# Kernel tuning notes

Measured on AMD Instinct MI355X. Metric: run time of the kernel, lower is better.

Reference implementation:

```python
import jax, jax.numpy as jnp
import numpy as np

U = 8192        # unique source nodes this hop
E = 200000      # candidate paths (edges)
D = 768         # node feature dim (== hidden, GIN residual requires it)
DE = 50         # edge one-hot dim
O = 768         # output dim
BN_EPS = 1e-5


def setup_inputs() -> dict:
    key = jax.random.key(0)
    ks = jax.random.split(key, 10)
    inp = {
        "x_src_unique": jax.random.normal(ks[0], (U, D), dtype=jnp.float32),
        "unique_src_to_process_indices": jnp.arange(U, dtype=jnp.int64),
        "path_source_indices_global": jax.random.randint(ks[1], (E,), 0, U).astype(jnp.int64),
        "path_target_node_features": jax.random.normal(ks[2], (E, D), dtype=jnp.float32),
        "path_edge_features": jax.random.normal(ks[3], (E, DE), dtype=jnp.float32),
        # edge_transform_linear: Linear(D+DE, H) with bias
        "W_edge": jax.random.normal(ks[4], (D, D + DE), dtype=jnp.float32) * (1.0 / np.sqrt(D + DE)),
        "b_edge": jnp.zeros((D,), dtype=jnp.float32),
        # MLP: two bias-free linears with BatchNorm1d between
        "W1": jax.random.normal(ks[5], (D, D), dtype=jnp.float32) * (1.0 / np.sqrt(D)),
        "W2": jax.random.normal(ks[6], (O, D), dtype=jnp.float32) * (1.0 / np.sqrt(D)),
        "bn_gamma": jnp.ones((D,), dtype=jnp.float32),
        "bn_beta": jnp.zeros((D,), dtype=jnp.float32),
        "eps_param": jnp.zeros((1,), dtype=jnp.float32),  # GIN eps (init_eps=0)
    }
    return inp


def reference(x_src_unique, unique_src_to_process_indices, path_source_indices_global,
              path_target_node_features, path_edge_features,
              W_edge, b_edge, W1, W2, bn_gamma, bn_beta, eps_param):
    # map global source ids -> local rows of x_src_unique (unique ids are sorted)
    local_idx = jnp.searchsorted(unique_src_to_process_indices, path_source_indices_global)

    # per-path message: relu(Linear([h_tgt ; e_onehot]))  -> [E, H]
    msg_in = jnp.concatenate([path_target_node_features, path_edge_features], axis=-1)
    msgs = jax.nn.relu(msg_in @ W_edge.T + b_edge)

    # scatter-sum messages to their source node  -> [U, H]
    agg = jax.ops.segment_sum(msgs, local_idx, num_segments=x_src_unique.shape[0])

    # GIN combine + MLP (BatchNorm1d in training mode, batch > 1)
    h = (1.0 + eps_param[0]) * x_src_unique + agg
    h1 = h @ W1.T                               # [U, H]
    mean = jnp.mean(h1, axis=0)
    var = jnp.var(h1, axis=0)                   # biased, matches torch BN normalization
    h1 = (h1 - mean) * jax.lax.rsqrt(var + BN_EPS) * bn_gamma + bn_beta
    h1 = jax.nn.relu(h1)
    return h1 @ W2.T                            # [U, O]
```

## Files before the change

kernel.cpp:

```cpp
#include <hip/hip_runtime.h>
#include <stdint.h>
#include <math.h>

typedef unsigned short u16;
typedef __attribute__((ext_vector_type(4))) float f32x4;
typedef __attribute__((ext_vector_type(8))) short s16x8;
typedef __attribute__((ext_vector_type(4))) int i32x4;

#define U_N 8192
#define E_N 200000
#define M_PAD 200192
#define D_N 768
#define DE_N 50
#define KP8 896
#define NTI8 7
#define BN_EPS 1e-5f

__device__ __forceinline__ u16 f2bf(float f) {
  union { float f; unsigned u; } v; v.f = f;
  return (u16)((v.u + 0x7fffu + ((v.u >> 16) & 1u)) >> 16);
}
__device__ __forceinline__ float bf2f(u16 v) {
  union { unsigned u; float f; } x; x.u = ((unsigned)v) << 16; return x.f;
}
__device__ __forceinline__ void gload16(const void* g, void* l) {
  __builtin_amdgcn_global_load_lds((const __attribute__((address_space(1))) void*)g,
                                   (__attribute__((address_space(3))) void*)l, 16, 0, 0);
}

__global__ void k_localidx(const int* __restrict__ uniq, const int* __restrict__ src,
                           int* __restrict__ lidx) {
  int e = blockIdx.x * 256 + threadIdx.x;
  if (e >= E_N) return;
  int v = src[e];
  int lo = 0, hi = U_N;
  while (lo < hi) { int mid = (lo + hi) >> 1; if (uniq[mid] < v) lo = mid + 1; else hi = mid; }
  lidx[e] = lo;
}

__global__ void k_hist(const int* __restrict__ lidx, int* __restrict__ counts) {
  int e = blockIdx.x * 256 + threadIdx.x;
  if (e < E_N) atomicAdd(&counts[lidx[e]], 1);
}

__global__ void k_scan(const int* __restrict__ counts, int* __restrict__ starts) {
  __shared__ int part[1024];
  const int t = threadIdx.x;
  const int base = t * 8;
  int loc[8]; int s = 0;
#pragma unroll
  for (int i = 0; i < 8; i++) { loc[i] = s; s += counts[base + i]; }
  part[t] = s; __syncthreads();
  for (int off = 1; off < 1024; off <<= 1) {
    int v = (t >= off) ? part[t - off] : 0;
    __syncthreads();
    part[t] += v;
    __syncthreads();
  }
  const int pre = (t == 0) ? 0 : part[t - 1];
#pragma unroll
  for (int i = 0; i < 8; i++) starts[base + i] = pre + loc[i];
  if (t == 1023) starts[8192] = pre + s;
}

__global__ void k_scatter(const int* __restrict__ lidx, const int* __restrict__ starts,
                          int* __restrict__ cursor, int* __restrict__ eord,
                          int* __restrict__ nsort) {
  int e = blockIdx.x * 256 + threadIdx.x;
  if (e >= E_N) return;
  int u = lidx[e];
  int pos = atomicAdd(&cursor[u], 1);
  eord[starts[u] + pos] = e;
  nsort[starts[u] + pos] = u;
}

__global__ __launch_bounds__(256)
void k_pack_q8(const float* __restrict__ tgt, const float* __restrict__ edg,
               const int* __restrict__ eord, char* __restrict__ Aq,
               float* __restrict__ sA) {
  const int row = blockIdx.x * 4 + (threadIdx.x >> 6);
  const int lane = threadIdx.x & 63;
  if (row >= E_N) return;
  const int e = eord[row];
  const int k0 = lane * 16;
  float v[16];
#pragma unroll
  for (int z = 0; z < 16; z++) v[z] = 0.f;
  if (k0 < D_N) {
    const f32x4* p = (const f32x4*)(tgt + (size_t)e * D_N + k0);
#pragma unroll
    for (int zz = 0; zz < 4; zz++) {
      const f32x4 f = p[zz];
#pragma unroll
      for (int b = 0; b < 4; b++) v[zz * 4 + b] = f[b];
    }
  } else if (k0 < KP8) {
#pragma unroll
    for (int z = 0; z < 16; z++) {
      const int kk = k0 + z - D_N;
      v[z] = (kk < DE_N) ? edg[(size_t)e * DE_N + kk] : 0.f;
    }
  }
  float am = 0.f;
#pragma unroll
  for (int z = 0; z < 16; z++) am = fmaxf(am, fabsf(v[z]));
#pragma unroll
  for (int off = 32; off > 0; off >>= 1) am = fmaxf(am, __shfl_xor(am, off));
  am = fmaxf(am, 1e-8f);
  const float inv = 127.f / am;
  if (lane == 0) sA[row] = am / 127.f;
  if (k0 < KP8) {
    int wq[4];
#pragma unroll
    for (int zz = 0; zz < 4; zz++) {
      int b0 = (int)rintf(fminf(fmaxf(v[zz*4+0] * inv, -127.f), 127.f));
      int b1 = (int)rintf(fminf(fmaxf(v[zz*4+1] * inv, -127.f), 127.f));
      int b2 = (int)rintf(fminf(fmaxf(v[zz*4+2] * inv, -127.f), 127.f));
      int b3 = (int)rintf(fminf(fmaxf(v[zz*4+3] * inv, -127.f), 127.f));
      wq[zz] = (b0 & 255) | ((b1 & 255) << 8) | ((b2 & 255) << 16) | (b3 << 24);
    }
    i32x4 out = {wq[0], wq[1], wq[2], wq[3]};
    *(i32x4*)(Aq + (size_t)row * KP8 + k0) = out;
  }
}

__global__ __launch_bounds__(256)
void k_convw_q8(const float* __restrict__ W, char* __restrict__ Wq,
                float* __restrict__ sW) {
  const int row = blockIdx.x * 4 + (threadIdx.x >> 6);
  const int lane = threadIdx.x & 63;
  if (row >= D_N) return;
  const int k0 = lane * 16;
  float v[16];
#pragma unroll
  for (int z = 0; z < 16; z++) v[z] = 0.f;
  if (k0 < KP8) {
#pragma unroll
    for (int z = 0; z < 16; z++) {
      const int kk = k0 + z;
      v[z] = (kk < D_N + DE_N) ? W[(size_t)row * (D_N + DE_N) + kk] : 0.f;
    }
  }
  float am = 0.f;
#pragma unroll
  for (int z = 0; z < 16; z++) am = fmaxf(am, fabsf(v[z]));
#pragma unroll
  for (int off = 32; off > 0; off >>= 1) am = fmaxf(am, __shfl_xor(am, off));
  am = fmaxf(am, 1e-8f);
  const float inv = 127.f / am;
  if (lane == 0) sW[row] = am / 127.f;
  if (k0 < KP8) {
    int wq[4];
#pragma unroll
    for (int zz = 0; zz < 4; zz++) {
      int b0 = (int)rintf(fminf(fmaxf(v[zz*4+0] * inv, -127.f), 127.f));
      int b1 = (int)rintf(fminf(fmaxf(v[zz*4+1] * inv, -127.f), 127.f));
      int b2 = (int)rintf(fminf(fmaxf(v[zz*4+2] * inv, -127.f), 127.f));
      int b3 = (int)rintf(fminf(fmaxf(v[zz*4+3] * inv, -127.f), 127.f));
      wq[zz] = (b0 & 255) | ((b1 & 255) << 8) | ((b2 & 255) << 16) | (b3 << 24);
    }
    i32x4 out = {wq[0], wq[1], wq[2], wq[3]};
    *(i32x4*)(Wq + (size_t)row * KP8 + k0) = out;
  }
}

__global__ void k_conv_w(const float* __restrict__ W, u16* __restrict__ Wb, int count) {
  int i = blockIdx.x * 256 + threadIdx.x;
  if (i < count) Wb[i] = f2bf(W[i]);
}

__global__ __launch_bounds__(512)
void gemm_edge8(const char* __restrict__ Aq, const char* __restrict__ Wq,
                const float* __restrict__ sA, const float* __restrict__ sW,
                const float* __restrict__ bias, const int* __restrict__ nsort,
                float* __restrict__ agg) {
  __shared__ char lds[139264];

  const int orig = blockIdx.x;
  const int xcd = orig & 7, i8_ = orig >> 3;
  const int wgid = (xcd < 2 ? xcd * 294 : 588 + (xcd - 2) * 293) + i8_;
  const int bm = (wgid / 3) * 256;
  const int bn = (wgid % 3) * 256;

  const int tid = threadIdx.x;
  const int w = tid >> 6, lane = tid & 63;
  const int wm = w >> 2, wn = w & 3;
  const int rl = lane & 15, K16 = lane >> 4;
  const int srr = lane >> 3;
  const int ssrc = (lane & 7) ^ srr;

  i32x4 acc[8][4] = {};

#define STAGE8(T)                                                                       \
  {                                                                                     \
    const int b_ = (T) & 1;                                                             \
    const int k0_ = (T) * 128;                                                          \
    _Pragma("unroll")                                                                   \
    for (int c_ = 0; c_ < 4; ++c_) {                                                    \
      const int cc_ = c_ * 8 + w;                                                       \
      const int r_ = cc_ * 8 + srr;                                                     \
      gload16(Aq + (size_t)(bm + r_) * KP8 + k0_ + ssrc * 16, lds + b_ * 32768 + cc_ * 1024); \
    }                                                                                   \
    _Pragma("unroll")                                                                   \
    for (int c_ = 0; c_ < 4; ++c_) {                                                    \
      const int cc_ = c_ * 8 + w;                                                       \
      const int r_ = cc_ * 8 + srr;                                                     \
      gload16(Wq + (size_t)(bn + r_) * KP8 + k0_ + ssrc * 16, lds + 65536 + b_ * 32768 + cc_ * 1024); \
    }                                                                                   \
  }

#define COMPUTE_H(BB, h_)                                                               \
  {                                                                                     \
    const char* Ab = lds + (BB) * 32768;                                                \
    const char* Bb = lds + 65536 + (BB) * 32768;                                        \
    const int sb_ = (h_) * 4 + K16;                                                     \
    const int sw_ = (sb_ ^ (rl & 7)) * 16;                                              \
    i32x4 bfr[4], af[4];                                                                \
    _Pragma("unroll")                                                                   \
    for (int j_ = 0; j_ < 4; ++j_)                                                      \
      bfr[j_] = *(const i32x4*)(Bb + (wn * 64 + j_ * 16 + rl) * 128 + sw_);             \
    _Pragma("unroll")                                                                   \
    for (int i_ = 0; i_ < 4; ++i_)                                                      \
      af[i_] = *(const i32x4*)(Ab + (wm * 128 + i_ * 16 + rl) * 128 + sw_);             \
    __builtin_amdgcn_s_setprio(1);                                                      \
    _Pragma("unroll")                                                                   \
    for (int i_ = 0; i_ < 4; ++i_)                                                      \
      _Pragma("unroll")                                                                 \
      for (int j_ = 0; j_ < 4; ++j_)                                                    \
        acc[i_][j_] = __builtin_amdgcn_mfma_i32_16x16x64_i8(af[i_], bfr[j_],            \
                                                            acc[i_][j_], 0, 0, 0);     \
    __builtin_amdgcn_s_setprio(0);                                                      \
    _Pragma("unroll")                                                                   \
    for (int i_ = 0; i_ < 4; ++i_)                                                      \
      af[i_] = *(const i32x4*)(Ab + (wm * 128 + (4 + i_) * 16 + rl) * 128 + sw_);       \
    __builtin_amdgcn_s_setprio(1);                                                      \
    _Pragma("unroll")                                                                   \
    for (int i_ = 0; i_ < 4; ++i_)                                                      \
      _Pragma("unroll")                                                                 \
      for (int j_ = 0; j_ < 4; ++j_)                                                    \
        acc[4 + i_][j_] = __builtin_amdgcn_mfma_i32_16x16x64_i8(af[i_], bfr[j_],        \
                                                                acc[4 + i_][j_], 0, 0, 0); \
    __builtin_amdgcn_s_setprio(0);                                                      \
  }

#define VMC(n)  asm volatile("s_waitcnt vmcnt(" #n ")" ::: "memory")
#define BAR()   __builtin_amdgcn_s_barrier()

  STAGE8(0)
  for (int t = 0; t < NTI8 - 1; ++t) {
    BAR();
    STAGE8(t + 1)
    VMC(8);
    BAR();
    asm volatile("" ::: "memory");
    COMPUTE_H(t & 1, 0)
    COMPUTE_H(t & 1, 1)
  }
  BAR();
  VMC(0);
  BAR();
  asm volatile("" ::: "memory");
  COMPUTE_H(0, 0)
  COMPUTE_H(0, 1)

#undef STAGE8
#undef COMPUTE_H

  BAR();

  u16* tile = (u16*)lds;
  int* nseg = (int*)(lds + 137216);
  float* sAl = (float*)(lds + 138240);
  for (int i = tid; i < 256; i += 512) {
    nseg[i] = nsort[bm + i];
    sAl[i] = sA[bm + i];
  }
  __syncthreads();

  const int rq = (lane >> 4) * 4;
  const int cl = lane & 15;
#pragma unroll
  for (int j = 0; j < 4; ++j) {
    const int col16 = wn * 64 + j * 16 + cl;
    const float swn = sW[bn + col16];
    const float bj = bias[bn + col16];
#pragma unroll
    for (int mf = 0; mf < 8; ++mf) {
      const int r0 = wm * 128 + mf * 16 + rq;
#pragma unroll
      for (int q = 0; q < 4; ++q) {
        const int r = r0 + q;
        const float v = fmaf((float)acc[mf][j][q], sAl[r] * swn, bj);
        tile[r * 268 + col16] = f2bf(v > 0.f ? v : 0.f);
      }
    }
  }
  __syncthreads();

  const int col = tid & 255;
  const int rbase = (tid >> 8) * 128;
  float s = 0.f;
  int cur = -1;
  for (int r = 0; r < 128; ++r) {
    const int nd = nseg[rbase + r];
    const float v = bf2f(tile[(rbase + r) * 268 + col]);
    if (nd != cur) {
      if (cur >= 0) atomicAdd(&agg[(size_t)cur * D_N + bn + col], s);
      s = 0.f;
      cur = nd;
    }
    if (nd >= 0) s += v;
  }
  if (cur >= 0) atomicAdd(&agg[(size_t)cur * D_N + bn + col], s);

#undef VMC
#undef BAR
}

__global__ void k_build_h(const float* __restrict__ x, const float* __restrict__ agg,
                          const float* __restrict__ epsp, u16* __restrict__ hbf) {
  int i = blockIdx.x * 256 + threadIdx.x;
  if (i >= U_N * D_N) return;
  float h = (1.f + epsp[0]) * x[i] + agg[i];
  hbf[i] = f2bf(h);
}

__global__ __launch_bounds__(256)
void gemm_h1(const u16* __restrict__ A, const u16* __restrict__ B,
             u16* __restrict__ h1b, float* __restrict__ ssum, float* __restrict__ ssq) {
  __shared__ u16 As[128 * 64];
  __shared__ u16 Bs[128 * 64];
  const int bm = (blockIdx.x / 6) * 128;
  const int bn = (blockIdx.x % 6) * 128;
  const int t = threadIdx.x;
  const int wave = t >> 6, lane = t & 63;
  const int wr = (wave & 1) * 64, wc = (wave >> 1) * 64;
  const int srow = lane >> 3, scol = (lane & 7) * 8;
  const int rl = lane & 15, kl = (lane >> 4) * 8;
  f32x4 acc[4][4] = {};
  for (int k0 = 0; k0 < D_N; k0 += 64) {
#pragma unroll
    for (int q = 0; q < 4; q++) {
      const int c = wave * 4 + q;
      const int row = c * 8 + srow;
      gload16(A + (size_t)(bm + row) * D_N + k0 + scol, As + c * 512);
      gload16(B + (size_t)(bn + row) * D_N + k0 + scol, Bs + c * 512);
    }
    __syncthreads();
#pragma unroll
    for (int ks = 0; ks < 2; ks++) {
      s16x8 af[4], bfr[4];
#pragma unroll
      for (int i = 0; i < 4; i++) af[i] = *(const s16x8*)&As[(wr + i * 16 + rl) * 64 + ks * 32 + kl];
#pragma unroll
      for (int j = 0; j < 4; j++) bfr[j] = *(const s16x8*)&Bs[(wc + j * 16 + rl) * 64 + ks * 32 + kl];
#pragma unroll
      for (int i = 0; i < 4; i++)
#pragma unroll
        for (int j = 0; j < 4; j++)
          acc[i][j] = __builtin_amdgcn_mfma_f32_16x16x32_bf16(af[i], bfr[j], acc[i][j], 0, 0, 0);
    }
    __syncthreads();
  }
  const int cl = lane & 15, rq = (lane >> 4) * 4;
#pragma unroll
  for (int j = 0; j < 4; j++) {
    const int n = bn + wc + j * 16 + cl;
    float cs = 0.f, cq = 0.f;
#pragma unroll
    for (int i = 0; i < 4; i++) {
      const int r = bm + wr + i * 16 + rq;
#pragma unroll
      for (int q = 0; q < 4; q++) {
        const float v = acc[i][j][q];
        cs += v; cq += v * v;
        h1b[(size_t)(r + q) * D_N + n] = f2bf(v);
      }
    }
    cs += __shfl_xor(cs, 16); cq += __shfl_xor(cq, 16);
    cs += __shfl_xor(cs, 32); cq += __shfl_xor(cq, 32);
    if (lane < 16) { atomicAdd(&ssum[n], cs); atomicAdd(&ssq[n], cq); }
  }
}

__global__ __launch_bounds__(256)
void gemm_bf16_g(const u16* __restrict__ A, const u16* __restrict__ B,
                 float* __restrict__ C, int ntn, int K) {
  __shared__ u16 As[128 * 64];
  __shared__ u16 Bs[128 * 64];
  const int bm = (blockIdx.x / ntn) * 128;
  const int bn = (blockIdx.x % ntn) * 128;
  const int t = threadIdx.x;
  const int wave = t >> 6, lane = t & 63;
  const int wr = (wave & 1) * 64, wc = (wave >> 1) * 64;
  const int srow = lane >> 3, scol = (lane & 7) * 8;
  const int rl = lane & 15, kl = (lane >> 4) * 8;
  const int N = ntn * 128;
  f32x4 acc[4][4] = {};
  for (int k0 = 0; k0 < K; k0 += 64) {
#pragma unroll
    for (int q = 0; q < 4; q++) {
      const int c = wave * 4 + q;
      const int row = c * 8 + srow;
      gload16(A + (size_t)(bm + row) * K + k0 + scol, As + c * 512);
      gload16(B + (size_t)(bn + row) * K + k0 + scol, Bs + c * 512);
    }
    __syncthreads();
#pragma unroll
    for (int ks = 0; ks < 2; ks++) {
      s16x8 af[4], bfr[4];
#pragma unroll
      for (int i = 0; i < 4; i++) af[i] = *(const s16x8*)&As[(wr + i * 16 + rl) * 64 + ks * 32 + kl];
#pragma unroll
      for (int j = 0; j < 4; j++) bfr[j] = *(const s16x8*)&Bs[(wc + j * 16 + rl) * 64 + ks * 32 + kl];
#pragma unroll
      for (int i = 0; i < 4; i++)
#pragma unroll
        for (int j = 0; j < 4; j++)
          acc[i][j] = __builtin_amdgcn_mfma_f32_16x16x32_bf16(af[i], bfr[j], acc[i][j], 0, 0, 0);
    }
    __syncthreads();
  }
  const int cl = lane & 15, rq = (lane >> 4) * 4;
#pragma unroll
  for (int i = 0; i < 4; i++)
#pragma unroll
    for (int j = 0; j < 4; j++) {
      const int n = bn + wc + j * 16 + cl;
      const int r = bm + wr + i * 16 + rq;
#pragma unroll
      for (int q = 0; q < 4; q++)
        C[(size_t)(r + q) * N + n] = acc[i][j][q];
    }
}

__global__ void k_bnfinal(const float* __restrict__ ssum, const float* __restrict__ ssq,
                          const float* __restrict__ gamma, const float* __restrict__ beta,
                          float* __restrict__ scale, float* __restrict__ shift) {
  int c = blockIdx.x * 256 + threadIdx.x;
  if (c >= D_N) return;
  double mean = (double)ssum[c] / (double)U_N;
  double var = (double)ssq[c] / (double)U_N - mean * mean;
  float sc = (float)((double)gamma[c] / sqrt(var + (double)BN_EPS));
  scale[c] = sc;
  shift[c] = beta[c] - (float)mean * sc;
}

__global__ void k_bnapply(const u16* __restrict__ h1b, const float* __restrict__ scale,
                          const float* __restrict__ shift, u16* __restrict__ h2) {
  int i = blockIdx.x * 256 + threadIdx.x;
  if (i >= U_N * D_N) return;
  int c = i % D_N;
  float v = bf2f(h1b[i]) * scale[c] + shift[c];
  h2[i] = f2bf(v > 0.f ? v : 0.f);
}

extern "C" void kernel_launch(void* const* d_in, const int* in_sizes, int n_in,
                              void* d_out, int out_size, void* d_ws, size_t ws_size,
                              hipStream_t stream) {
  const float* x     = (const float*)d_in[0];
  const int*   uniq  = (const int*)d_in[1];
  const int*   srcg  = (const int*)d_in[2];
  const float* tgt   = (const float*)d_in[3];
  const float* edg   = (const float*)d_in[4];
  const float* Wedge = (const float*)d_in[5];
  const float* bedge = (const float*)d_in[6];
  const float* W1    = (const float*)d_in[7];
  const float* W2    = (const float*)d_in[8];
  const float* gamma = (const float*)d_in[9];
  const float* beta  = (const float*)d_in[10];
  const float* epsp  = (const float*)d_in[11];
  float* out = (float*)d_out;
  char* ws = (char*)d_ws;

  char*  Aq    = (char*) (ws + 0);
  float* agg   = (float*)(ws + 179372032ull);
  u16*   h1b   = (u16*)  (ws + 204537856ull);
  u16*   hbf   = (u16*)  (ws + 217120768ull);
  u16*   h2b   = (u16*)  (ws + 229703680ull);
  char*  Wq    = (char*) (ws + 242286592ull);
  u16*   w1b   = (u16*)  (ws + 242974720ull);
  u16*   w2b   = (u16*)  (ws + 244154368ull);
  float* sA    = (float*)(ws + 245334016ull);
  float* sW    = (float*)(ws + 246134784ull);
  int*   lidx  = (int*)  (ws + 246138880ull);
  int*   eord  = (int*)  (ws + 246938880ull);
  int*   nsort = (int*)  (ws + 247738880ull);
  int*   counts= (int*)  (ws + 248539648ull);
  int*   cursor= (int*)  (ws + 248572416ull);
  int*   starts= (int*)  (ws + 248605184ull);
  float* ssum  = (float*)(ws + 248638208ull);
  float* ssq   = (float*)(ws + 248641280ull);
  float* scale = (float*)(ws + 248644352ull);
  float* shift = (float*)(ws + 248647424ull);

  hipMemsetAsync(counts, 0, 65536, stream);
  hipMemsetAsync(ssum, 0, 2 * D_N * 4, stream);
  hipMemsetAsync(agg, 0, (size_t)U_N * D_N * 4, stream);
  hipMemsetAsync(nsort + E_N, 0xFF, (M_PAD - E_N) * 4, stream);

  k_convw_q8<<<D_N / 4, 256, 0, stream>>>(Wedge, Wq, sW);
  k_conv_w<<<(D_N * D_N + 255) / 256, 256, 0, stream>>>(W1, w1b, D_N * D_N);
  k_conv_w<<<(D_N * D_N + 255) / 256, 256, 0, stream>>>(W2, w2b, D_N * D_N);

  k_localidx<<<(E_N + 255) / 256, 256, 0, stream>>>(uniq, srcg, lidx);
  k_hist<<<(E_N + 255) / 256, 256, 0, stream>>>(lidx, counts);
  k_scan<<<1, 1024, 0, stream>>>(counts, starts);
  k_scatter<<<(E_N + 255) / 256, 256, 0, stream>>>(lidx, starts, cursor, eord, nsort);

  k_pack_q8<<<E_N / 4, 256, 0, stream>>>(tgt, edg, eord, Aq, sA);

  gemm_edge8<<<782 * 3, 512, 0, stream>>>(Aq, Wq, sA, sW, bedge, nsort, agg);

  k_build_h<<<(U_N * D_N + 255) / 256, 256, 0, stream>>>(x, agg, epsp, hbf);

  gemm_h1<<<(U_N / 128) * 6, 256, 0, stream>>>(hbf, w1b, h1b, ssum, ssq);

  k_bnfinal<<<3, 256, 0, stream>>>(ssum, ssq, gamma, beta, scale, shift);
  k_bnapply<<<(U_N * D_N + 255) / 256, 256, 0, stream>>>(h1b, scale, shift, h2b);

  gemm_bf16_g<<<(U_N / 128) * 6, 256, 0, stream>>>(h2b, w2b, out, 6, D_N);
}
```

Before: 569.1 us.

## Retile int8 edge GEMM to 128x128x64 with K padded to 832, fuse small kernels

```diff
diff --git a/kernel.cpp b/kernel.cpp
--- a/kernel.cpp
+++ b/kernel.cpp
@@ -9,11 +9,12 @@
 
 #define U_N 8192
 #define E_N 200000
-#define M_PAD 200192
+#define M_PAD 200064
+#define NMT 1563
 #define D_N 768
 #define DE_N 50
-#define KP8 896
-#define NTI8 7
+#define KP_E 832
+#define NTI 13
 #define BN_EPS 1e-5f
 
 __device__ __forceinline__ u16 f2bf(float f) {
@@ -28,19 +29,15 @@
                                    (__attribute__((address_space(3))) void*)l, 16, 0, 0);
 }
 
-__global__ void k_localidx(const int* __restrict__ uniq, const int* __restrict__ src,
-                           int* __restrict__ lidx) {
+__global__ void k_lh(const int* __restrict__ uniq, const int* __restrict__ src,
+                     int* __restrict__ lidx, int* __restrict__ counts) {
   int e = blockIdx.x * 256 + threadIdx.x;
   if (e >= E_N) return;
   int v = src[e];
   int lo = 0, hi = U_N;
   while (lo < hi) { int mid = (lo + hi) >> 1; if (uniq[mid] < v) lo = mid + 1; else hi = mid; }
   lidx[e] = lo;
-}
-
-__global__ void k_hist(const int* __restrict__ lidx, int* __restrict__ counts) {
-  int e = blockIdx.x * 256 + threadIdx.x;
-  if (e < E_N) atomicAdd(&counts[lidx[e]], 1);
+  atomicAdd(&counts[lo], 1);
 }
 
 __global__ void k_scan(const int* __restrict__ counts, int* __restrict__ starts) {
@@ -94,7 +91,7 @@
 #pragma unroll
       for (int b = 0; b < 4; b++) v[zz * 4 + b] = f[b];
     }
-  } else if (k0 < KP8) {
+  } else if (k0 < KP_E) {
 #pragma unroll
     for (int z = 0; z < 16; z++) {
       const int kk = k0 + z - D_N;
@@ -109,7 +106,7 @@
   am = fmaxf(am, 1e-8f);
   const float inv = 127.f / am;
   if (lane == 0) sA[row] = am / 127.f;
-  if (k0 < KP8) {
+  if (k0 < KP_E) {
     int wq[4];
 #pragma unroll
     for (int zz = 0; zz < 4; zz++) {
@@ -120,7 +117,7 @@
       wq[zz] = (b0 & 255) | ((b1 & 255) << 8) | ((b2 & 255) << 16) | (b3 << 24);
     }
     i32x4 out = {wq[0], wq[1], wq[2], wq[3]};
-    *(i32x4*)(Aq + (size_t)row * KP8 + k0) = out;
+    *(i32x4*)(Aq + (size_t)row * KP_E + k0) = out;
   }
 }
 
@@ -134,7 +131,7 @@
   float v[16];
 #pragma unroll
   for (int z = 0; z < 16; z++) v[z] = 0.f;
-  if (k0 < KP8) {
+  if (k0 < KP_E) {
 #pragma unroll
     for (int z = 0; z < 16; z++) {
       const int kk = k0 + z;
@@ -149,7 +146,7 @@
   am = fmaxf(am, 1e-8f);
   const float inv = 127.f / am;
   if (lane == 0) sW[row] = am / 127.f;
-  if (k0 < KP8) {
+  if (k0 < KP_E) {
     int wq[4];
 #pragma unroll
     for (int zz = 0; zz < 4; zz++) {
@@ -160,68 +157,65 @@
       wq[zz] = (b0 & 255) | ((b1 & 255) << 8) | ((b2 & 255) << 16) | (b3 << 24);
     }
     i32x4 out = {wq[0], wq[1], wq[2], wq[3]};
-    *(i32x4*)(Wq + (size_t)row * KP8 + k0) = out;
-  }
-}
-
-__global__ void k_conv_w(const float* __restrict__ W, u16* __restrict__ Wb, int count) {
+    *(i32x4*)(Wq + (size_t)row * KP_E + k0) = out;
+  }
+}
+
+__global__ void k_conv_w2(const float* __restrict__ W1, const float* __restrict__ W2,
+                          u16* __restrict__ w1b, u16* __restrict__ w2b) {
   int i = blockIdx.x * 256 + threadIdx.x;
-  if (i < count) Wb[i] = f2bf(W[i]);
-}
-
-__global__ __launch_bounds__(512)
-void gemm_edge8(const char* __restrict__ Aq, const char* __restrict__ Wq,
+  const int C = D_N * D_N;
+  if (i < C) w1b[i] = f2bf(W1[i]);
+  else if (i < 2 * C) w2b[i - C] = f2bf(W2[i - C]);
+}
+
+__global__ __launch_bounds__(256, 4)
+void gemm_edge9(const char* __restrict__ Aq, const char* __restrict__ Wq,
                 const float* __restrict__ sA, const float* __restrict__ sW,
                 const float* __restrict__ bias, const int* __restrict__ nsort,
                 float* __restrict__ agg) {
-  __shared__ char lds[139264];
+  __shared__ char lds[34816];
 
   const int orig = blockIdx.x;
   const int xcd = orig & 7, i8_ = orig >> 3;
-  const int wgid = (xcd < 2 ? xcd * 294 : 588 + (xcd - 2) * 293) + i8_;
-  const int bm = (wgid / 3) * 256;
-  const int bn = (wgid % 3) * 256;
+  const int wgid = (xcd < 2 ? xcd * 1173 : 2346 + (xcd - 2) * 1172) + i8_;
+  const int bm = (wgid / 6) * 128;
+  const int bn = (wgid % 6) * 128;
 
   const int tid = threadIdx.x;
   const int w = tid >> 6, lane = tid & 63;
-  const int wm = w >> 2, wn = w & 3;
+  const int wm = w & 1, wn = w >> 1;
   const int rl = lane & 15, K16 = lane >> 4;
-  const int srr = lane >> 3;
-  const int ssrc = (lane & 7) ^ srr;
-
-  i32x4 acc[8][4] = {};
-
-#define STAGE8(T)                                                                       \
+  const int sws = (K16 ^ ((rl >> 1) & 3)) * 16;
+  const int srow = tid >> 2;
+  const int sg0 = (tid & 3) ^ ((srow >> 1) & 3);
+
+  i32x4 acc[4][4] = {};
+
+#define VMC(n)  asm volatile("s_waitcnt vmcnt(" #n ")" ::: "memory")
+#define BAR()   __builtin_amdgcn_s_barrier()
+
+#define STAGE9(T)                                                                       \
   {                                                                                     \
     const int b_ = (T) & 1;                                                             \
-    const int k0_ = (T) * 128;                                                          \
-    _Pragma("unroll")                                                                   \
-    for (int c_ = 0; c_ < 4; ++c_) {                                                    \
-      const int cc_ = c_ * 8 + w;                                                       \
-      const int r_ = cc_ * 8 + srr;                                                     \
-      gload16(Aq + (size_t)(bm + r_) * KP8 + k0_ + ssrc * 16, lds + b_ * 32768 + cc_ * 1024); \
-    }                                                                                   \
-    _Pragma("unroll")                                                                   \
-    for (int c_ = 0; c_ < 4; ++c_) {                                                    \
-      const int cc_ = c_ * 8 + w;                                                       \
-      const int r_ = cc_ * 8 + srr;                                                     \
-      gload16(Wq + (size_t)(bn + r_) * KP8 + k0_ + ssrc * 16, lds + 65536 + b_ * 32768 + cc_ * 1024); \
-    }                                                                                   \
-  }
-
-#define COMPUTE_H(BB, h_)                                                               \
+    const int k0_ = (T) * 64;                                                           \
+    gload16(Aq + (size_t)(bm + srow) * KP_E + k0_ + sg0 * 16, lds + b_ * 16384 + tid * 16); \
+    gload16(Aq + (size_t)(bm + srow + 64) * KP_E + k0_ + sg0 * 16, lds + b_ * 16384 + 4096 + tid * 16); \
+    gload16(Wq + (size_t)(bn + srow) * KP_E + k0_ + sg0 * 16, lds + b_ * 16384 + 8192 + tid * 16); \
+    gload16(Wq + (size_t)(bn + srow + 64) * KP_E + k0_ + sg0 * 16, lds + b_ * 16384 + 12288 + tid * 16); \
+  }
+
+#define COMPUTE9(BB)                                                                    \
   {                                                                                     \
-    const char* Ab = lds + (BB) * 32768;                                                \
-    const char* Bb = lds + 65536 + (BB) * 32768;                                        \
-    const int sb_ = (h_) * 4 + K16;                                                     \
-    const int sw_ = (sb_ ^ (rl & 7)) * 16;                                              \
-    i32x4 bfr[4], af[4];                                                                \
+    const char* Ab = lds + (BB) * 16384;                                                \
+    const char* Bb = Ab + 8192;                                                         \
+    i32x4 af[4], bfr[4];                                                                \
     _Pragma("unroll")                                                                   \
     for (int j_ = 0; j_ < 4; ++j_)                                                      \
-      bfr[j_] = *(const i32x4*)(Bb + (wn * 64 + j_ * 16 + rl) * 128 + sw_);             \
+      bfr[j_] = *(const i32x4*)(Bb + (wn * 64 + j_ * 16 + rl) * 64 + sws);              \
     _Pragma("unroll")                                                                   \
     for (int i_ = 0; i_ < 4; ++i_)                                                      \
-      af[i_] = *(const i32x4*)(Ab + (wm * 128 + i_ * 16 + rl) * 128 + sw_);             \
+      af[i_] = *(const i32x4*)(Ab + (wm * 64 + i_ * 16 + rl) * 64 + sws);               \
     __builtin_amdgcn_s_setprio(1);                                                      \
     _Pragma("unroll")                                                                   \
     for (int i_ = 0; i_ < 4; ++i_)                                                      \
@@ -230,48 +224,32 @@
         acc[i_][j_] = __builtin_amdgcn_mfma_i32_16x16x64_i8(af[i_], bfr[j_],            \
                                                             acc[i_][j_], 0, 0, 0);     \
     __builtin_amdgcn_s_setprio(0);                                                      \
-    _Pragma("unroll")                                                                   \
-    for (int i_ = 0; i_ < 4; ++i_)                                                      \
-      af[i_] = *(const i32x4*)(Ab + (wm * 128 + (4 + i_) * 16 + rl) * 128 + sw_);       \
-    __builtin_amdgcn_s_setprio(1);                                                      \
-    _Pragma("unroll")                                                                   \
-    for (int i_ = 0; i_ < 4; ++i_)                                                      \
-      _Pragma("unroll")                                                                 \
-      for (int j_ = 0; j_ < 4; ++j_)                                                    \
-        acc[4 + i_][j_] = __builtin_amdgcn_mfma_i32_16x16x64_i8(af[i_], bfr[j_],        \
-                                                                acc[4 + i_][j_], 0, 0, 0); \
-    __builtin_amdgcn_s_setprio(0);                                                      \
-  }
-
-#define VMC(n)  asm volatile("s_waitcnt vmcnt(" #n ")" ::: "memory")
-#define BAR()   __builtin_amdgcn_s_barrier()
-
-  STAGE8(0)
-  for (int t = 0; t < NTI8 - 1; ++t) {
+  }
+
+  STAGE9(0)
+  for (int t = 0; t < NTI - 1; ++t) {
     BAR();
-    STAGE8(t + 1)
-    VMC(8);
+    STAGE9(t + 1)
+    VMC(4);
     BAR();
     asm volatile("" ::: "memory");
-    COMPUTE_H(t & 1, 0)
-    COMPUTE_H(t & 1, 1)
+    COMPUTE9(t & 1)
   }
   BAR();
   VMC(0);
   BAR();
   asm volatile("" ::: "memory");
-  COMPUTE_H(0, 0)
-  COMPUTE_H(0, 1)
-
-#undef STAGE8
-#undef COMPUTE_H
+  COMPUTE9(0)
+
+#undef STAGE9
+#undef COMPUTE9
 
   BAR();
 
   u16* tile = (u16*)lds;
-  int* nseg = (int*)(lds + 137216);
-  float* sAl = (float*)(lds + 138240);
-  for (int i = tid; i < 256; i += 512) {
+  int* nseg = (int*)(lds + 33792);
+  float* sAl = (float*)(lds + 34304);
+  for (int i = tid; i < 128; i += 256) {
     nseg[i] = nsort[bm + i];
     sAl[i] = sA[bm + i];
   }
@@ -285,25 +263,25 @@
     const float swn = sW[bn + col16];
     const float bj = bias[bn + col16];
 #pragma unroll
-    for (int mf = 0; mf < 8; ++mf) {
-      const int r0 = wm * 128 + mf * 16 + rq;
+    for (int i = 0; i < 4; ++i) {
+      const int r0 = wm * 64 + i * 16 + rq;
 #pragma unroll
       for (int q = 0; q < 4; ++q) {
         const int r = r0 + q;
-        const float v = fmaf((float)acc[mf][j][q], sAl[r] * swn, bj);
-        tile[r * 268 + col16] = f2bf(v > 0.f ? v : 0.f);
+        const float v = fmaf((float)acc[i][j][q], sAl[r] * swn, bj);
+        tile[r * 132 + col16] = f2bf(v > 0.f ? v : 0.f);
       }
     }
   }
   __syncthreads();
 
-  const int col = tid & 255;
-  const int rbase = (tid >> 8) * 128;
+  const int col = tid & 127;
+  const int rbase = (tid >> 7) * 64;
   float s = 0.f;
   int cur = -1;
-  for (int r = 0; r < 128; ++r) {
+  for (int r = 0; r < 64; ++r) {
     const int nd = nseg[rbase + r];
-    const float v = bf2f(tile[(rbase + r) * 268 + col]);
+    const float v = bf2f(tile[(rbase + r) * 132 + col]);
     if (nd != cur) {
       if (cur >= 0) atomicAdd(&agg[(size_t)cur * D_N + bn + col], s);
       s = 0.f;
@@ -474,25 +452,25 @@
   char* ws = (char*)d_ws;
 
   char*  Aq    = (char*) (ws + 0);
-  float* agg   = (float*)(ws + 179372032ull);
-  u16*   h1b   = (u16*)  (ws + 204537856ull);
-  u16*   hbf   = (u16*)  (ws + 217120768ull);
-  u16*   h2b   = (u16*)  (ws + 229703680ull);
-  char*  Wq    = (char*) (ws + 242286592ull);
-  u16*   w1b   = (u16*)  (ws + 242974720ull);
-  u16*   w2b   = (u16*)  (ws + 244154368ull);
-  float* sA    = (float*)(ws + 245334016ull);
-  float* sW    = (float*)(ws + 246134784ull);
-  int*   lidx  = (int*)  (ws + 246138880ull);
-  int*   eord  = (int*)  (ws + 246938880ull);
-  int*   nsort = (int*)  (ws + 247738880ull);
-  int*   counts= (int*)  (ws + 248539648ull);
-  int*   cursor= (int*)  (ws + 248572416ull);
-  int*   starts= (int*)  (ws + 248605184ull);
-  float* ssum  = (float*)(ws + 248638208ull);
-  float* ssq   = (float*)(ws + 248641280ull);
-  float* scale = (float*)(ws + 248644352ull);
-  float* shift = (float*)(ws + 248647424ull);
+  float* agg   = (float*)(ws + 166454272ull);
+  u16*   h1b   = (u16*)  (ws + 191620096ull);
+  u16*   hbf   = (u16*)  (ws + 204203008ull);
+  u16*   h2b   = (u16*)  (ws + 216785920ull);
+  char*  Wq    = (char*) (ws + 229368832ull);
+  u16*   w1b   = (u16*)  (ws + 230007808ull);
+  u16*   w2b   = (u16*)  (ws + 231187456ull);
+  float* sA    = (float*)(ws + 232367104ull);
+  float* sW    = (float*)(ws + 233167872ull);
+  int*   lidx  = (int*)  (ws + 233171968ull);
+  int*   eord  = (int*)  (ws + 233971968ull);
+  int*   nsort = (int*)  (ws + 234771968ull);
+  int*   counts= (int*)  (ws + 235572736ull);
+  int*   cursor= (int*)  (ws + 235605504ull);
+  int*   starts= (int*)  (ws + 235638272ull);
+  float* ssum  = (float*)(ws + 235671296ull);
+  float* ssq   = (float*)(ws + 235674368ull);
+  float* scale = (float*)(ws + 235677440ull);
+  float* shift = (float*)(ws + 235680512ull);
 
   hipMemsetAsync(counts, 0, 65536, stream);
   hipMemsetAsync(ssum, 0, 2 * D_N * 4, stream);
@@ -500,17 +478,15 @@
   hipMemsetAsync(nsort + E_N, 0xFF, (M_PAD - E_N) * 4, stream);
 
   k_convw_q8<<<D_N / 4, 256, 0, stream>>>(Wedge, Wq, sW);
-  k_conv_w<<<(D_N * D_N + 255) / 256, 256, 0, stream>>>(W1, w1b, D_N * D_N);
-  k_conv_w<<<(D_N * D_N + 255) / 256, 256, 0, stream>>>(W2, w2b, D_N * D_N);
-
-  k_localidx<<<(E_N + 255) / 256, 256, 0, stream>>>(uniq, srcg, lidx);
-  k_hist<<<(E_N + 255) / 256, 256, 0, stream>>>(lidx, counts);
+  k_conv_w2<<<(2 * D_N * D_N + 255) / 256, 256, 0, stream>>>(W1, W2, w1b, w2b);
+
+  k_lh<<<(E_N + 255) / 256, 256, 0, stream>>>(uniq, srcg, lidx, counts);
   k_scan<<<1, 1024, 0, stream>>>(counts, starts);
   k_scatter<<<(E_N + 255) / 256, 256, 0, stream>>>(lidx, starts, cursor, eord, nsort);
 
   k_pack_q8<<<E_N / 4, 256, 0, stream>>>(tgt, edg, eord, Aq, sA);
 
-  gemm_edge8<<<782 * 3, 512, 0, stream>>>(Aq, Wq, sA, sW, bedge, nsort, agg);
+  gemm_edge9<<<NMT * 6, 256, 0, stream>>>(Aq, Wq, sA, sW, bedge, nsort, agg);
 
   k_build_h<<<(U_N * D_N + 255) / 256, 256, 0, stream>>>(x, agg, epsp, hbf);
 
```

Measured after the change: 500.9 us. 12.0% less time.
